# Kernel optimization log

Hardware: AMD Instinct MI355X
Metric: run time of the kernel (lower is better)

## Reference

```python
import jax, jax.numpy as jnp
import numpy as np


def setup_inputs() -> dict:
    key = jax.random.key(0)
    k1, k2, k3, k4, k5 = jax.random.split(key, 5)
    B, N, E, C, O = 4, 10000, 32, 128, 128
    x = jax.random.normal(k1, (B, N, C), dtype=jnp.float32)
    idx = jax.random.randint(k2, (B, N, E), 0, N)
    drop = jax.random.uniform(k3, (B, N, E)) < 0.1
    edge_index = jnp.where(drop, -1, idx).astype(jnp.int64)
    W = jax.random.normal(k4, (2 * C, O), dtype=jnp.float32) * (1.0 / np.sqrt(2 * C))
    b = jax.random.normal(k5, (O,), dtype=jnp.float32) * 0.01
    return {"x": x, "edge_index": edge_index, "W": W, "b": b}


def reference(x, edge_index, W, b):
    B, N, C = x.shape
    E = edge_index.shape[-1]
    # pad a zero node row; -1 indices point at it (torch negative-index semantics)
    padded = jnp.concatenate([x, jnp.zeros((B, 1, C), dtype=x.dtype)], axis=1)  # [B, N+1, C]
    idx = jnp.where(edge_index < 0, N, edge_index)
    neigh = jax.vmap(lambda p, i: p[i])(padded, idx)  # [B, N, E, C]
    x_e = jnp.broadcast_to(x[:, :, None, :], (B, N, E, C))
    feat = jnp.concatenate([x_e, neigh - x_e], axis=-1)  # [B, N, E, 2C]
    h = jax.nn.elu(jnp.einsum('bnec,co->bneo', feat, W) + b)  # [B, N, E, O]
    h = jnp.where((edge_index != -1)[..., None], h, -jnp.inf)
    return jnp.max(h, axis=2)  # [B, N, O]
```

## Files before the change

kernel.cpp:

```cpp
#include <hip/hip_runtime.h>
#include <math.h>

#define BATCH 4
#define NNODE 10000
#define EDIM  32
#define CDIM  128
#define ODIM  128
#define MTOT  (BATCH * NNODE)

typedef __attribute__((ext_vector_type(8))) short bf16x8;
typedef __attribute__((ext_vector_type(4))) float f32x4;

__device__ __forceinline__ unsigned short f2bf(float f) {
    unsigned u = __float_as_uint(f);
    u += 0x7fffu + ((u >> 16) & 1u);
    return (unsigned short)(u >> 16);
}

__global__ __launch_bounds__(256) void prep_w(
    const float* __restrict__ W, unsigned short* __restrict__ Bcat,
    unsigned short* __restrict__ Tsent)
{
    int gid = blockIdx.x * 256 + threadIdx.x;
    int n = gid >> 7;
    int k = gid & 127;
    float v;
    if (n < 128) v = W[(size_t)k * ODIM + n] - W[(size_t)(k + 128) * ODIM + n];
    else         v = W[(size_t)(k + 128) * ODIM + (n - 128)];
    Bcat[(size_t)n * CDIM + k] = f2bf(v);
    if (gid < ODIM) Tsent[gid] = 0xFF80;
}

__global__ __launch_bounds__(256) void gemm_mfma(
    const float* __restrict__ x,
    const unsigned short* __restrict__ Bcat,
    const float* __restrict__ bias,
    float* __restrict__ U,
    unsigned short* __restrict__ T)
{
    __shared__ unsigned short As[64 * 128];

    const int tid  = threadIdx.x;
    const int m0   = blockIdx.x * 64;
    const int wv   = tid >> 6;
    const int lane = tid & 63;
    const int l16  = lane & 15;
    const int quad = lane >> 4;
    const int nq   = wv * 64;

    #pragma unroll
    for (int i = 0; i < 8; i++) {
        int lin = i * 256 + tid;
        int row = lin >> 5;
        int f4  = lin & 31;
        float4 v = *(const float4*)&x[(size_t)(m0 + row) * CDIM + f4 * 4];
        ushort4 h;
        h.x = f2bf(v.x); h.y = f2bf(v.y); h.z = f2bf(v.z); h.w = f2bf(v.w);
        int kblk = f4 >> 1, half = f4 & 1;
        *(ushort4*)((char*)As + row * 256 + (((kblk ^ (row & 15)) << 4) + half * 8)) = h;
    }
    __syncthreads();

    f32x4 acc[4][4];
    #pragma unroll
    for (int i = 0; i < 4; i++)
        #pragma unroll
        for (int j = 0; j < 4; j++) acc[i][j] = (f32x4){0.f, 0.f, 0.f, 0.f};

    #pragma unroll
    for (int ks = 0; ks < 4; ks++) {
        const int kb = ks * 32 + quad * 8;

        bf16x8 bfr[4];
        #pragma unroll
        for (int ct = 0; ct < 4; ct++)
            bfr[ct] = *(const bf16x8*)(Bcat + (size_t)(nq + ct * 16 + l16) * CDIM + kb);

        bf16x8 afr[4];
        #pragma unroll
        for (int rt = 0; rt < 4; rt++) {
            int row  = rt * 16 + l16;
            int kblk = ks * 4 + quad;
            afr[rt] = *(const bf16x8*)((char*)As + row * 256 + ((kblk ^ l16) << 4));
        }

        #pragma unroll
        for (int rt = 0; rt < 4; rt++)
            #pragma unroll
            for (int ct = 0; ct < 4; ct++)
                acc[rt][ct] = __builtin_amdgcn_mfma_f32_16x16x32_bf16(
                    afr[rt], bfr[ct], acc[rt][ct], 0, 0, 0);
    }

    if (wv < 2) {
        #pragma unroll
        for (int ct = 0; ct < 4; ct++) {
            int n = nq + ct * 16 + l16;
            float bb = bias[n];
            #pragma unroll
            for (int rt = 0; rt < 4; rt++) {
                int row = m0 + rt * 16 + quad * 4;
                #pragma unroll
                for (int r = 0; r < 4; r++)
                    U[(size_t)(row + r) * ODIM + n] = acc[rt][ct][r] + bb;
            }
        }
    } else {
        #pragma unroll
        for (int ct = 0; ct < 4; ct++) {
            int n = nq - 128 + ct * 16 + l16;
            #pragma unroll
            for (int rt = 0; rt < 4; rt++) {
                int row = m0 + rt * 16 + quad * 4;
                #pragma unroll
                for (int r = 0; r < 4; r++)
                    T[(size_t)(row + r) * ODIM + n] = f2bf(acc[rt][ct][r]);
            }
        }
    }
}

__global__ __launch_bounds__(256) void gather_max(
    const int* __restrict__ idx,
    const float* Uin,
    const unsigned short* __restrict__ T,
    float* out)
{
    __shared__ int sidx[16][EDIM];

    const int g   = blockIdx.x;
    const int b   = g & 3;
    const int nb0 = (g >> 2) * 16;
    const int tid = threadIdx.x;
    const int sent = NNODE * (BATCH - b);

    #pragma unroll
    for (int i = 0; i < 2; i++) {
        int lin = i * 256 + tid;
        int n = lin >> 5, e = lin & 31;
        int j = idx[(size_t)(b * NNODE + nb0 + n) * EDIM + e];
        sidx[n][e] = (j < 0) ? sent : j;
    }
    __syncthreads();

    const int wv   = tid >> 6;
    const int lane = tid & 63;
    const int q4   = lane >> 4;
    const int l16  = lane & 15;
    const int myn  = wv * 4 + q4;
    const int node = b * NNODE + nb0 + myn;
    const unsigned short* tb = T + (size_t)b * NNODE * ODIM;
    const int o8 = l16 * 8;

    float m[8];
    #pragma unroll
    for (int i = 0; i < 8; i++) m[i] = -INFINITY;

    #pragma unroll
    for (int e0 = 0; e0 < EDIM; e0 += 8) {
        uint4 v[8];
        #pragma unroll
        for (int q = 0; q < 8; q++) {
            int j = sidx[myn][e0 + q];
            v[q] = *(const uint4*)(tb + (size_t)j * ODIM + o8);
        }
        #pragma unroll
        for (int q = 0; q < 8; q++) {
            m[0] = fmaxf(m[0], __uint_as_float(v[q].x << 16));
            m[1] = fmaxf(m[1], __uint_as_float(v[q].x & 0xffff0000u));
            m[2] = fmaxf(m[2], __uint_as_float(v[q].y << 16));
            m[3] = fmaxf(m[3], __uint_as_float(v[q].y & 0xffff0000u));
            m[4] = fmaxf(m[4], __uint_as_float(v[q].z << 16));
            m[5] = fmaxf(m[5], __uint_as_float(v[q].z & 0xffff0000u));
            m[6] = fmaxf(m[6], __uint_as_float(v[q].w << 16));
            m[7] = fmaxf(m[7], __uint_as_float(v[q].w & 0xffff0000u));
        }
    }

    const bool any = m[0] > -INFINITY;
    float4 u0 = *(const float4*)&Uin[(size_t)node * ODIM + o8];
    float4 u1 = *(const float4*)&Uin[(size_t)node * ODIM + o8 + 4];
    float uu[8] = {u0.x, u0.y, u0.z, u0.w, u1.x, u1.y, u1.z, u1.w};
    float r[8];
    #pragma unroll
    for (int i = 0; i < 8; i++) {
        float s = uu[i] + m[i];
        r[i] = any ? (s > 0.f ? s : __expf(s) - 1.f) : -INFINITY;
    }
    float4 w0 = make_float4(r[0], r[1], r[2], r[3]);
    float4 w1 = make_float4(r[4], r[5], r[6], r[7]);
    *(float4*)&out[(size_t)node * ODIM + o8]     = w0;
    *(float4*)&out[(size_t)node * ODIM + o8 + 4] = w1;
}

extern "C" void kernel_launch(void* const* d_in, const int* in_sizes, int n_in,
                              void* d_out, int out_size, void* d_ws, size_t ws_size,
                              hipStream_t stream) {
    const float* x    = (const float*)d_in[0];
    const int*   idx  = (const int*)d_in[1];
    const float* W    = (const float*)d_in[2];
    const float* bias = (const float*)d_in[3];
    float* out        = (float*)d_out;

    const size_t tBytes = (size_t)(MTOT + 1) * ODIM * sizeof(unsigned short);
    const size_t uBytes = (size_t)MTOT * ODIM * sizeof(float);
    const size_t bBytes = (size_t)256 * CDIM * sizeof(unsigned short);
    unsigned short* T = (unsigned short*)d_ws;
    float* U;
    unsigned short* Bcat;
    if (ws_size >= tBytes + uBytes + bBytes) {
        U    = (float*)((char*)d_ws + tBytes);
        Bcat = (unsigned short*)((char*)d_ws + tBytes + uBytes);
    } else {
        U    = out;
        Bcat = (unsigned short*)((char*)d_ws + tBytes);
    }
    unsigned short* Tsent = T + (size_t)MTOT * ODIM;

    prep_w    <<<128,        256, 0, stream>>>(W, Bcat, Tsent);
    gemm_mfma <<<MTOT / 64,  256, 0, stream>>>(x, Bcat, bias, U, T);
    gather_max<<<MTOT / 16,  256, 0, stream>>>(idx, U, T, out);
}
```

Baseline: 110.4 us.

## Store U in bf16, stage GEMM epilogue through LDS, deepen gather batching

The intermediate U tensor is now stored as bf16 instead of fp32, which halves its write and read traffic. The GEMM epilogue is staged through LDS so that U and T are written as coalesced row-contiguous ushort4 stores instead of scattered 2-byte or 4-byte writes. The GEMM tile shrinks to 32 rows per block, giving more blocks, and the gather issues 16 neighbour loads per batch instead of 8 to increase memory-level parallelism. The cost is lower precision for U and extra LDS passes and barriers in the GEMM.

```diff
diff --git a/kernel.cpp b/kernel.cpp
--- a/kernel.cpp
+++ b/kernel.cpp
@@ -15,6 +15,9 @@
     unsigned u = __float_as_uint(f);
     u += 0x7fffu + ((u >> 16) & 1u);
     return (unsigned short)(u >> 16);
+}
+__device__ __forceinline__ float bf2f(unsigned short h) {
+    return __uint_as_float(((unsigned)h) << 16);
 }
 
 __global__ __launch_bounds__(256) void prep_w(
@@ -35,13 +38,15 @@
     const float* __restrict__ x,
     const unsigned short* __restrict__ Bcat,
     const float* __restrict__ bias,
-    float* __restrict__ U,
+    unsigned short* __restrict__ U,
     unsigned short* __restrict__ T)
 {
-    __shared__ unsigned short As[64 * 128];
+    __shared__ char lds_raw[32 * 132 * 4];
+    unsigned short* As = (unsigned short*)lds_raw;
+    float*          Cf = (float*)lds_raw;
 
     const int tid  = threadIdx.x;
-    const int m0   = blockIdx.x * 64;
+    const int m0   = blockIdx.x * 32;
     const int wv   = tid >> 6;
     const int lane = tid & 63;
     const int l16  = lane & 15;
@@ -49,7 +54,7 @@
     const int nq   = wv * 64;
 
     #pragma unroll
-    for (int i = 0; i < 8; i++) {
+    for (int i = 0; i < 4; i++) {
         int lin = i * 256 + tid;
         int row = lin >> 5;
         int f4  = lin & 31;
@@ -61,9 +66,9 @@
     }
     __syncthreads();
 
-    f32x4 acc[4][4];
-    #pragma unroll
-    for (int i = 0; i < 4; i++)
+    f32x4 acc[2][4];
+    #pragma unroll
+    for (int i = 0; i < 2; i++)
         #pragma unroll
         for (int j = 0; j < 4; j++) acc[i][j] = (f32x4){0.f, 0.f, 0.f, 0.f};
 
@@ -76,55 +81,71 @@
         for (int ct = 0; ct < 4; ct++)
             bfr[ct] = *(const bf16x8*)(Bcat + (size_t)(nq + ct * 16 + l16) * CDIM + kb);
 
-        bf16x8 afr[4];
-        #pragma unroll
-        for (int rt = 0; rt < 4; rt++) {
+        bf16x8 afr[2];
+        #pragma unroll
+        for (int rt = 0; rt < 2; rt++) {
             int row  = rt * 16 + l16;
             int kblk = ks * 4 + quad;
             afr[rt] = *(const bf16x8*)((char*)As + row * 256 + ((kblk ^ l16) << 4));
         }
 
         #pragma unroll
-        for (int rt = 0; rt < 4; rt++)
+        for (int rt = 0; rt < 2; rt++)
             #pragma unroll
             for (int ct = 0; ct < 4; ct++)
                 acc[rt][ct] = __builtin_amdgcn_mfma_f32_16x16x32_bf16(
                     afr[rt], bfr[ct], acc[rt][ct], 0, 0, 0);
     }
 
+    __syncthreads();
     if (wv < 2) {
         #pragma unroll
-        for (int ct = 0; ct < 4; ct++) {
-            int n = nq + ct * 16 + l16;
-            float bb = bias[n];
+        for (int rt = 0; rt < 2; rt++)
             #pragma unroll
-            for (int rt = 0; rt < 4; rt++) {
-                int row = m0 + rt * 16 + quad * 4;
+            for (int ct = 0; ct < 4; ct++)
                 #pragma unroll
                 for (int r = 0; r < 4; r++)
-                    U[(size_t)(row + r) * ODIM + n] = acc[rt][ct][r] + bb;
-            }
-        }
-    } else {
-        #pragma unroll
-        for (int ct = 0; ct < 4; ct++) {
-            int n = nq - 128 + ct * 16 + l16;
+                    Cf[(rt * 16 + quad * 4 + r) * 132 + nq + ct * 16 + l16] = acc[rt][ct][r];
+    }
+    __syncthreads();
+    #pragma unroll
+    for (int i = 0; i < 4; i++) {
+        int lin = i * 256 + tid;
+        int row = lin >> 5, f4 = lin & 31;
+        float4 v  = *(const float4*)&Cf[row * 132 + f4 * 4];
+        float4 bb = *(const float4*)&bias[f4 * 4];
+        ushort4 h;
+        h.x = f2bf(v.x + bb.x); h.y = f2bf(v.y + bb.y);
+        h.z = f2bf(v.z + bb.z); h.w = f2bf(v.w + bb.w);
+        *(ushort4*)&U[(size_t)(m0 + row) * ODIM + f4 * 4] = h;
+    }
+    __syncthreads();
+    if (wv >= 2) {
+        #pragma unroll
+        for (int rt = 0; rt < 2; rt++)
             #pragma unroll
-            for (int rt = 0; rt < 4; rt++) {
-                int row = m0 + rt * 16 + quad * 4;
+            for (int ct = 0; ct < 4; ct++)
                 #pragma unroll
                 for (int r = 0; r < 4; r++)
-                    T[(size_t)(row + r) * ODIM + n] = f2bf(acc[rt][ct][r]);
-            }
-        }
+                    Cf[(rt * 16 + quad * 4 + r) * 132 + (nq - 128) + ct * 16 + l16] = acc[rt][ct][r];
+    }
+    __syncthreads();
+    #pragma unroll
+    for (int i = 0; i < 4; i++) {
+        int lin = i * 256 + tid;
+        int row = lin >> 5, f4 = lin & 31;
+        float4 v = *(const float4*)&Cf[row * 132 + f4 * 4];
+        ushort4 h;
+        h.x = f2bf(v.x); h.y = f2bf(v.y); h.z = f2bf(v.z); h.w = f2bf(v.w);
+        *(ushort4*)&T[(size_t)(m0 + row) * ODIM + f4 * 4] = h;
     }
 }
 
 __global__ __launch_bounds__(256) void gather_max(
     const int* __restrict__ idx,
-    const float* Uin,
+    const unsigned short* __restrict__ Ub,
     const unsigned short* __restrict__ T,
-    float* out)
+    float* __restrict__ out)
 {
     __shared__ int sidx[16][EDIM];
 
@@ -152,20 +173,22 @@
     const unsigned short* tb = T + (size_t)b * NNODE * ODIM;
     const int o8 = l16 * 8;
 
+    uint4 uraw = *(const uint4*)(Ub + (size_t)node * ODIM + o8);
+
     float m[8];
     #pragma unroll
     for (int i = 0; i < 8; i++) m[i] = -INFINITY;
 
     #pragma unroll
-    for (int e0 = 0; e0 < EDIM; e0 += 8) {
-        uint4 v[8];
-        #pragma unroll
-        for (int q = 0; q < 8; q++) {
+    for (int e0 = 0; e0 < EDIM; e0 += 16) {
+        uint4 v[16];
+        #pragma unroll
+        for (int q = 0; q < 16; q++) {
             int j = sidx[myn][e0 + q];
             v[q] = *(const uint4*)(tb + (size_t)j * ODIM + o8);
         }
         #pragma unroll
-        for (int q = 0; q < 8; q++) {
+        for (int q = 0; q < 16; q++) {
             m[0] = fmaxf(m[0], __uint_as_float(v[q].x << 16));
             m[1] = fmaxf(m[1], __uint_as_float(v[q].x & 0xffff0000u));
             m[2] = fmaxf(m[2], __uint_as_float(v[q].y << 16));
@@ -178,19 +201,19 @@
     }
 
     const bool any = m[0] > -INFINITY;
-    float4 u0 = *(const float4*)&Uin[(size_t)node * ODIM + o8];
-    float4 u1 = *(const float4*)&Uin[(size_t)node * ODIM + o8 + 4];
-    float uu[8] = {u0.x, u0.y, u0.z, u0.w, u1.x, u1.y, u1.z, u1.w};
+    float uu[8];
+    uu[0] = bf2f((unsigned short)(uraw.x & 0xffff)); uu[1] = bf2f((unsigned short)(uraw.x >> 16));
+    uu[2] = bf2f((unsigned short)(uraw.y & 0xffff)); uu[3] = bf2f((unsigned short)(uraw.y >> 16));
+    uu[4] = bf2f((unsigned short)(uraw.z & 0xffff)); uu[5] = bf2f((unsigned short)(uraw.z >> 16));
+    uu[6] = bf2f((unsigned short)(uraw.w & 0xffff)); uu[7] = bf2f((unsigned short)(uraw.w >> 16));
     float r[8];
     #pragma unroll
     for (int i = 0; i < 8; i++) {
         float s = uu[i] + m[i];
         r[i] = any ? (s > 0.f ? s : __expf(s) - 1.f) : -INFINITY;
     }
-    float4 w0 = make_float4(r[0], r[1], r[2], r[3]);
-    float4 w1 = make_float4(r[4], r[5], r[6], r[7]);
-    *(float4*)&out[(size_t)node * ODIM + o8]     = w0;
-    *(float4*)&out[(size_t)node * ODIM + o8 + 4] = w1;
+    *(float4*)&out[(size_t)node * ODIM + o8]     = make_float4(r[0], r[1], r[2], r[3]);
+    *(float4*)&out[(size_t)node * ODIM + o8 + 4] = make_float4(r[4], r[5], r[6], r[7]);
 }
 
 extern "C" void kernel_launch(void* const* d_in, const int* in_sizes, int n_in,
@@ -203,21 +226,13 @@
     float* out        = (float*)d_out;
 
     const size_t tBytes = (size_t)(MTOT + 1) * ODIM * sizeof(unsigned short);
-    const size_t uBytes = (size_t)MTOT * ODIM * sizeof(float);
-    const size_t bBytes = (size_t)256 * CDIM * sizeof(unsigned short);
-    unsigned short* T = (unsigned short*)d_ws;
-    float* U;
-    unsigned short* Bcat;
-    if (ws_size >= tBytes + uBytes + bBytes) {
-        U    = (float*)((char*)d_ws + tBytes);
-        Bcat = (unsigned short*)((char*)d_ws + tBytes + uBytes);
-    } else {
-        U    = out;
-        Bcat = (unsigned short*)((char*)d_ws + tBytes);
-    }
+    const size_t uBytes = (size_t)MTOT * ODIM * sizeof(unsigned short);
+    unsigned short* T    = (unsigned short*)d_ws;
+    unsigned short* U    = (unsigned short*)((char*)d_ws + tBytes);
+    unsigned short* Bcat = (unsigned short*)((char*)d_ws + tBytes + uBytes);
     unsigned short* Tsent = T + (size_t)MTOT * ODIM;
 
     prep_w    <<<128,        256, 0, stream>>>(W, Bcat, Tsent);
-    gemm_mfma <<<MTOT / 64,  256, 0, stream>>>(x, Bcat, bias, U, T);
+    gemm_mfma <<<MTOT / 32,  256, 0, stream>>>(x, Bcat, bias, U, T);
     gather_max<<<MTOT / 16,  256, 0, stream>>>(idx, U, T, out);
 }
```

Measured after the change: 111.3 us. About the same (+0.8%).
